# Optimization experiments

Measured on AMD Instinct MI355X. Metric: run time of the kernel, lower is better.

The kernel has to match this reference:

```python
import jax, jax.numpy as jnp
import numpy as np

# dims
B, L, D, H, HD, V, FF, NL = 1, 1024, 1024, 16, 64, 32000, 2816, 2
THETA = 500000.0
EPS = 1e-5
BOI, EOI = 31998, 31999
NEG = jnp.float32(-1e30)  # stands in for -inf in the additive mask


def setup_inputs() -> dict:
    key = jax.random.key(0)
    ks = jax.random.split(key, 12)
    tokens = jax.random.randint(ks[0], (B, L), 0, 31998)
    # inject two well-formed image spans per sequence (boi .. eoi)
    tokens = tokens.at[:, 100].set(BOI).at[:, 300].set(EOI)
    tokens = tokens.at[:, 500].set(BOI).at[:, 800].set(EOI)
    s = 0.02
    n = lambda k, shape: (jax.random.normal(k, shape, jnp.float32) * s)
    return {
        "tokens": tokens,
        "tok_emb": n(ks[1], (V, D)),
        "wq": n(ks[2], (NL, D, D)),
        "wk": n(ks[3], (NL, D, D)),
        "wv": n(ks[4], (NL, D, D)),
        "wo": n(ks[5], (NL, D, D)),
        "w1": n(ks[6], (NL, FF, D)),
        "w2": n(ks[7], (NL, D, FF)),
        "w3": n(ks[8], (NL, FF, D)),
        "attn_norm_w": jnp.ones((NL, D), jnp.float32),
        "ffn_norm_w": jnp.ones((NL, D), jnp.float32),
        "final_norm_w": jnp.ones((D,), jnp.float32),
        "w_out": n(ks[9], (V, D)),
    }


def rmsnorm(x, w):
    xf = x.astype(jnp.float32)
    y = xf * jax.lax.rsqrt(jnp.mean(xf * xf, axis=-1, keepdims=True) + EPS)
    return y.astype(x.dtype) * w


def rope_cos_sin():
    inv = 1.0 / (THETA ** (jnp.arange(0, HD, 2, dtype=jnp.float32) / HD))  # [HD/2]
    ang = jnp.arange(L, dtype=jnp.float32)[:, None] * inv[None, :]        # [L, HD/2]
    return jnp.cos(ang), jnp.sin(ang)


def apply_rope(x, cos, sin):
    # x: [B, L, H, HD]; pairs (even, odd) rotated by complex freqs_cis
    xr = x.astype(jnp.float32).reshape(B, L, H, HD // 2, 2)
    xe, xo = xr[..., 0], xr[..., 1]
    c = cos[None, :, None, :]
    s = sin[None, :, None, :]
    out = jnp.stack([xe * c - xo * s, xe * s + xo * c], axis=-1).reshape(B, L, H, HD)
    return out.astype(x.dtype)


def transfusion_mask(tokens):
    # causal everywhere + fully bidirectional within each boi..eoi span
    is_boi = tokens == BOI
    is_eoi = tokens == EOI
    boi_cnt = jnp.cumsum(is_boi.astype(jnp.int32), axis=1)          # inclusive
    eoi_before = jnp.cumsum(is_eoi.astype(jnp.int32), axis=1) - is_eoi.astype(jnp.int32)
    in_span = boi_cnt > eoi_before                                   # [B, L]
    same_span = (in_span[:, :, None] & in_span[:, None, :]) & (
        boi_cnt[:, :, None] == boi_cnt[:, None, :]
    )
    causal = jnp.arange(L)[:, None] >= jnp.arange(L)[None, :]        # [L, L]
    allowed = causal[None] | same_span                                # [B, L, L]
    return jnp.where(allowed, jnp.float32(0.0), NEG)


def reference(tokens, tok_emb, wq, wk, wv, wo, w1, w2, w3,
              attn_norm_w, ffn_norm_w, final_norm_w, w_out):
    h = tok_emb[tokens]                                # [B, L, D]
    cos, sin = rope_cos_sin()
    mask = transfusion_mask(tokens)[:, None]           # [B, 1, L, L]
    scale = 1.0 / jnp.sqrt(jnp.float32(HD))
    for l in range(NL):
        xn = rmsnorm(h, attn_norm_w[l])
        q = (xn @ wq[l].T).reshape(B, L, H, HD)
        k = (xn @ wk[l].T).reshape(B, L, H, HD)
        v = (xn @ wv[l].T).reshape(B, L, H, HD)
        q = apply_rope(q, cos, sin)
        k = apply_rope(k, cos, sin)
        q, k, v = (t.transpose(0, 2, 1, 3) for t in (q, k, v))  # [B, H, L, HD]
        scores = jnp.einsum("bhqd,bhkd->bhqk", q, k) * scale + mask
        p = jax.nn.softmax(scores.astype(jnp.float32), axis=-1).astype(q.dtype)
        attn = jnp.einsum("bhqk,bhkd->bhqd", p, v)
        attn = attn.transpose(0, 2, 1, 3).reshape(B, L, D)
        h = h + attn @ wo[l].T
        xn = rmsnorm(h, ffn_norm_w[l])
        h = h + (jax.nn.silu(xn @ w1[l].T) * (xn @ w3[l].T)) @ w2[l].T
    logits = rmsnorm(h, final_norm_w) @ w_out.T        # [B, L, V]
    return logits
```

## Files before the change

### kernel.cpp

```cpp
#include <hip/hip_runtime.h>
#include <hip/hip_bf16.h>
#include <stdint.h>

typedef unsigned short u16;
typedef __bf16 bf16x8 __attribute__((ext_vector_type(8)));
typedef u16 u16x8 __attribute__((ext_vector_type(8)));
typedef float f32x4 __attribute__((ext_vector_type(4)));

#define SEQ   1024
#define DM    1024
#define NHEADS 16
#define HDIM  64
#define VOC   32000
#define FFD   2816
#define NLAY  2

__device__ __forceinline__ u16 f2b(float f) {
    unsigned x = __builtin_bit_cast(unsigned, f);
    unsigned r = x + 0x7fffu + ((x >> 16) & 1u);
    return (u16)(r >> 16);
}
__device__ __forceinline__ float b2f(u16 u) {
    unsigned x = ((unsigned)u) << 16;
    return __builtin_bit_cast(float, x);
}
__device__ __forceinline__ float grpmax16(float v) {
    v = fmaxf(v, __shfl_xor(v, 1)); v = fmaxf(v, __shfl_xor(v, 2));
    v = fmaxf(v, __shfl_xor(v, 4)); v = fmaxf(v, __shfl_xor(v, 8));
    return v;
}
__device__ __forceinline__ float grpsum16(float v) {
    v += __shfl_xor(v, 1); v += __shfl_xor(v, 2);
    v += __shfl_xor(v, 4); v += __shfl_xor(v, 8);
    return v;
}

__device__ __forceinline__ void gll16(const void* g, void* l) {
    __builtin_amdgcn_global_load_lds(
        (__attribute__((address_space(1))) void*)(uintptr_t)g,
        (__attribute__((address_space(3))) void*)(uint32_t)(uintptr_t)l,
        16, 0, 0);
}
template <int N> __device__ __forceinline__ void vwait() {
    if constexpr (N == 0)       asm volatile("s_waitcnt vmcnt(0)" ::: "memory");
    else if constexpr (N == 4)  asm volatile("s_waitcnt vmcnt(4)" ::: "memory");
    else if constexpr (N == 8)  asm volatile("s_waitcnt vmcnt(8)" ::: "memory");
    else if constexpr (N == 10) asm volatile("s_waitcnt vmcnt(10)" ::: "memory");
    else if constexpr (N == 16) asm volatile("s_waitcnt vmcnt(16)" ::: "memory");
}
__device__ __forceinline__ int xcd_swz(int bid, int nwg) {
    const int q = nwg >> 3, r = nwg & 7;
    const int xcd = bid & 7, j = bid >> 3;
    const int start = (xcd < r) ? xcd * (q + 1) : r * (q + 1) + (xcd - r) * q;
    return start + j;
}

struct CvtArgs { const float* s[8]; u16* d[8]; int cum[9]; };
__global__ __launch_bounds__(256) void cvt_all_kernel(CvtArgs a) {
    const int stride = gridDim.x * 256;
    const int total = a.cum[8];
    for (int u = blockIdx.x * 256 + threadIdx.x; u < total; u += stride) {
        int g = 0;
#pragma unroll
        for (int k = 1; k < 8; ++k) g += (u >= a.cum[k]) ? 1 : 0;
        const int local = u - a.cum[g];
        const float4* sp = (const float4*)a.s[g] + (size_t)local * 4;
        const float4 x0 = sp[0], x1 = sp[1], x2 = sp[2], x3 = sp[3];
        ushort4 p0, p1, p2, p3;
        p0.x = f2b(x0.x); p0.y = f2b(x0.y); p0.z = f2b(x0.z); p0.w = f2b(x0.w);
        p1.x = f2b(x1.x); p1.y = f2b(x1.y); p1.z = f2b(x1.z); p1.w = f2b(x1.w);
        p2.x = f2b(x2.x); p2.y = f2b(x2.y); p2.z = f2b(x2.z); p2.w = f2b(x2.w);
        p3.x = f2b(x3.x); p3.y = f2b(x3.y); p3.z = f2b(x3.z); p3.w = f2b(x3.w);
        ushort4* dp = (ushort4*)a.d[g] + (size_t)local * 4;
        dp[0] = p0; dp[1] = p1; dp[2] = p2; dp[3] = p3;
    }
}

__global__ __launch_bounds__(256) void embed_kernel(const int* __restrict__ tok,
    const float* __restrict__ emb, float* __restrict__ h) {
    const int l = blockIdx.x;
    const int t = tok[l];
    ((float4*)(h + (size_t)l * DM))[threadIdx.x] =
        ((const float4*)(emb + (size_t)t * DM))[threadIdx.x];
}

__global__ __launch_bounds__(256) void ropetab_kernel(float* __restrict__ cosb,
                                                      float* __restrict__ sinb) {
    const int idx = blockIdx.x * 256 + threadIdx.x;
    const int l = idx >> 5, j = idx & 31;
    const float inv = __expf(-((float)j * (1.0f / 32.0f)) * 13.122363377404328f);
    const float ang = (float)l * inv;
    cosb[idx] = cosf(ang);
    sinb[idx] = sinf(ang);
}

__global__ void span_kernel(const int* __restrict__ tok, int* __restrict__ span,
                            int* __restrict__ tmask) {
    __shared__ int sb[SEQ], se[SEQ];
    __shared__ int tm[SEQ / 64];
    const int t = threadIdx.x;
    const int v = tok[t];
    const int bo = (v == 31998) ? 1 : 0;
    const int eo = (v == 31999) ? 1 : 0;
    sb[t] = bo; se[t] = eo;
    if (t < SEQ / 64) tm[t] = 0;
    __syncthreads();
    for (int o = 1; o < SEQ; o <<= 1) {
        int a = 0, b = 0;
        if (t >= o) { a = sb[t - o]; b = se[t - o]; }
        __syncthreads();
        sb[t] += a; se[t] += b;
        __syncthreads();
    }
    const int bc = sb[t];
    const int ec = se[t] - eo;
    const int id = (bc > ec) ? bc : 0;
    span[t] = id;
    if (id > 0) atomicOr(&tm[t >> 6], 1 << ((id - 1) & 31));
    __syncthreads();
    if (t < SEQ / 64) tmask[t] = tm[t];
}

__global__ __launch_bounds__(256) void rmsnorm_kernel(const float* __restrict__ x,
    const float* __restrict__ w, u16* __restrict__ o) {
    const int row = blockIdx.x;
    const float4 xv = ((const float4*)(x + (size_t)row * DM))[threadIdx.x];
    float ss = xv.x * xv.x + xv.y * xv.y + xv.z * xv.z + xv.w * xv.w;
    for (int off = 32; off; off >>= 1) ss += __shfl_xor(ss, off);
    __shared__ float red[4];
    const int lane = threadIdx.x & 63, wvi = threadIdx.x >> 6;
    if (lane == 0) red[wvi] = ss;
    __syncthreads();
    const float tot = red[0] + red[1] + red[2] + red[3];
    const float sc = rsqrtf(tot * (1.0f / (float)DM) + 1e-5f);
    const float4 wv4 = ((const float4*)w)[threadIdx.x];
    ushort4 ov;
    ov.x = f2b(xv.x * sc * wv4.x);
    ov.y = f2b(xv.y * sc * wv4.y);
    ov.z = f2b(xv.z * sc * wv4.z);
    ov.w = f2b(xv.w * sc * wv4.w);
    ((ushort4*)(o + (size_t)row * DM))[threadIdx.x] = ov;
}


template <int RESID, int BM, int BN>
__global__ __launch_bounds__(256) void gemm_p_kernel(const u16* __restrict__ A,
    const u16* __restrict__ B, float* __restrict__ C, const float* __restrict__ res,
    int N, int K) {
    constexpr int AL = BM / 32, BL = BN / 32, LOADS = AL + BL;
    constexpr int MF = BM / 32, NF = BN / 32;
    __shared__ __align__(16) u16 sA[2][BM * 64];
    __shared__ __align__(16) u16 sB[2][BN * 64];
    const int nwg = gridDim.x * gridDim.y;
    const int lid = xcd_swz(blockIdx.y * gridDim.x + blockIdx.x, nwg);
    const int tm = (lid % gridDim.x) * BM, tn = (lid / gridDim.x) * BN;
    const int tid = threadIdx.x, lane = tid & 63, wid = tid >> 6;
    const int wm = wid >> 1, wn = wid & 1, fr = lane & 15, g = lane >> 4;

    const u16* ap[AL]; const u16* bp[BL];
#pragma unroll
    for (int j = 0; j < AL; ++j) {
        const int idx = j * 256 + tid, r = idx >> 3, gr = (idx & 7) ^ (r & 7);
        ap[j] = A + (size_t)(tm + r) * K + gr * 8;
    }
#pragma unroll
    for (int j = 0; j < BL; ++j) {
        const int idx = j * 256 + tid, r = idx >> 3, gr = (idx & 7) ^ (r & 7);
        bp[j] = B + (size_t)(tn + r) * K + gr * 8;
    }

    f32x4 acc[MF][NF] = {};
    const int NT = K >> 6;
#pragma unroll
    for (int j = 0; j < AL; ++j) gll16(ap[j], &sA[0][(j * 256 + tid) * 8]);
#pragma unroll
    for (int j = 0; j < BL; ++j) gll16(bp[j], &sB[0][(j * 256 + tid) * 8]);

    int p = 0;
    for (int t = 0; t < NT; ++t) {
        if (t + 1 < NT) {
#pragma unroll
            for (int j = 0; j < AL; ++j) gll16(ap[j] + (t + 1) * 64, &sA[p ^ 1][(j * 256 + tid) * 8]);
#pragma unroll
            for (int j = 0; j < BL; ++j) gll16(bp[j] + (t + 1) * 64, &sB[p ^ 1][(j * 256 + tid) * 8]);
            vwait<LOADS>();
        } else {
            vwait<0>();
        }
        __builtin_amdgcn_s_barrier();
        __builtin_amdgcn_sched_barrier(0);
        bf16x8 af[MF][2], bfv[NF][2];
#pragma unroll
        for (int m = 0; m < MF; ++m)
#pragma unroll
            for (int ks = 0; ks < 2; ++ks) {
                const int row = wm * (BM / 2) + m * 16 + fr;
                const int gr = (ks * 4 + g) ^ (row & 7);
                af[m][ks] = *(const bf16x8*)&sA[p][row * 64 + gr * 8];
            }
#pragma unroll
        for (int n = 0; n < NF; ++n)
#pragma unroll
            for (int ks = 0; ks < 2; ++ks) {
                const int row = wn * (BN / 2) + n * 16 + fr;
                const int gr = (ks * 4 + g) ^ (row & 7);
                bfv[n][ks] = *(const bf16x8*)&sB[p][row * 64 + gr * 8];
            }
        __builtin_amdgcn_s_setprio(1);
#pragma unroll
        for (int m = 0; m < MF; ++m)
#pragma unroll
            for (int n = 0; n < NF; ++n)
#pragma unroll
                for (int ks = 0; ks < 2; ++ks)
                    acc[m][n] = __builtin_amdgcn_mfma_f32_16x16x32_bf16(af[m][ks], bfv[n][ks], acc[m][n], 0, 0, 0);
        __builtin_amdgcn_s_setprio(0);
        __builtin_amdgcn_s_barrier();
        p ^= 1;
    }

    const int cr = (lane >> 4) * 4, cc = lane & 15;
#pragma unroll
    for (int m = 0; m < MF; ++m)
#pragma unroll
        for (int n = 0; n < NF; ++n) {
            const int row0 = tm + wm * (BM / 2) + m * 16 + cr;
            const int col = tn + wn * (BN / 2) + n * 16 + cc;
#pragma unroll
            for (int r = 0; r < 4; ++r) {
                const size_t idx = (size_t)(row0 + r) * N + col;
                float v = acc[m][n][r];
                if (RESID) v += res[idx];
                C[idx] = v;
            }
        }
}

template <int RESID>
__global__ __launch_bounds__(512, 2) void gemm_big_kernel(const u16* __restrict__ A,
    const u16* __restrict__ B, float* __restrict__ C, const float* __restrict__ res,
    int N, int K) {
    __shared__ __align__(16) u16 sA[2][256 * 64];
    __shared__ __align__(16) u16 sB[2][256 * 64];
    const int nwg = gridDim.x * gridDim.y;
    const int lid = xcd_swz(blockIdx.y * gridDim.x + blockIdx.x, nwg);
    const int tm = (lid % gridDim.x) * 256;
    const int tn = (lid / gridDim.x) * 256;
    const int tid = threadIdx.x, lane = tid & 63, wid = tid >> 6;
    const int wm = wid >> 2, wn = wid & 3;
    const int fr = lane & 15, g = lane >> 4;

    const u16* ap[4]; const u16* bp[4];
#pragma unroll
    for (int j = 0; j < 4; ++j) {
        const int idx = j * 512 + tid, r = idx >> 3, gr = (idx & 7) ^ (r & 7);
        ap[j] = A + (size_t)(tm + r) * K + gr * 8;
        bp[j] = B + (size_t)(tn + r) * K + gr * 8;
    }

    f32x4 acc[8][4] = {};
    const int NT = K >> 6;
#pragma unroll
    for (int j = 0; j < 4; ++j) gll16(ap[j], &sA[0][(j * 512 + tid) * 8]);
#pragma unroll
    for (int j = 0; j < 4; ++j) gll16(bp[j], &sB[0][(j * 512 + tid) * 8]);

    int p = 0;
    for (int t = 0; t < NT; ++t) {
        if (t + 1 < NT) {
#pragma unroll
            for (int j = 0; j < 4; ++j) gll16(ap[j] + (t + 1) * 64, &sA[p ^ 1][(j * 512 + tid) * 8]);
#pragma unroll
            for (int j = 0; j < 4; ++j) gll16(bp[j] + (t + 1) * 64, &sB[p ^ 1][(j * 512 + tid) * 8]);
            vwait<8>();
        } else {
            vwait<0>();
        }
        __builtin_amdgcn_s_barrier();
        __builtin_amdgcn_sched_barrier(0);
        bf16x8 bfv[4][2];
#pragma unroll
        for (int mq = 0; mq < 4; ++mq) {
            if (mq == 0) {
#pragma unroll
                for (int n = 0; n < 4; ++n)
#pragma unroll
                    for (int ks = 0; ks < 2; ++ks) {
                        const int row = wn * 64 + n * 16 + fr;
                        const int gr = (ks * 4 + g) ^ (row & 7);
                        bfv[n][ks] = *(const bf16x8*)&sB[p][row * 64 + gr * 8];
                    }
            }
            bf16x8 af[2][2];
#pragma unroll
            for (int i = 0; i < 2; ++i)
#pragma unroll
                for (int ks = 0; ks < 2; ++ks) {
                    const int row = wm * 128 + (mq * 2 + i) * 16 + fr;
                    const int gr = (ks * 4 + g) ^ (row & 7);
                    af[i][ks] = *(const bf16x8*)&sA[p][row * 64 + gr * 8];
                }
            __builtin_amdgcn_s_setprio(1);
#pragma unroll
            for (int i = 0; i < 2; ++i)
#pragma unroll
                for (int n = 0; n < 4; ++n)
#pragma unroll
                    for (int ks = 0; ks < 2; ++ks)
                        acc[mq * 2 + i][n] = __builtin_amdgcn_mfma_f32_16x16x32_bf16(
                            af[i][ks], bfv[n][ks], acc[mq * 2 + i][n], 0, 0, 0);
            __builtin_amdgcn_s_setprio(0);
            __builtin_amdgcn_s_barrier();
        }
        p ^= 1;
    }

    const int cr = (lane >> 4) * 4, cc = lane & 15;
#pragma unroll
    for (int m = 0; m < 8; ++m)
#pragma unroll
        for (int n = 0; n < 4; ++n) {
            const int row0 = tm + wm * 128 + m * 16 + cr;
            const int col = tn + wn * 64 + n * 16 + cc;
#pragma unroll
            for (int r = 0; r < 4; ++r) {
                const size_t idx = (size_t)(row0 + r) * N + col;
                float v = acc[m][n][r];
                if (RESID) v += res[idx];
                C[idx] = v;
            }
        }
}

__global__ __launch_bounds__(256) void qkv_kernel(const u16* __restrict__ A,
    const u16* __restrict__ Bq, const u16* __restrict__ Bk, const u16* __restrict__ Bv,
    const float* __restrict__ cosb, const float* __restrict__ sinb,
    u16* __restrict__ qb, u16* __restrict__ kb, u16* __restrict__ vb) {
    __shared__ __align__(16) u16 sA[2][128 * 64];
    __shared__ __align__(16) u16 sB[2][128 * 64];
    const int lid = xcd_swz(blockIdx.y * gridDim.x + blockIdx.x, 8 * 24);
    const int tm = (lid % 8) * 128;
    const int yy = lid / 8;
    const int mat = yy >> 3;
    const int tn = (yy & 7) * 128;
    const u16* B = (mat == 0) ? Bq : (mat == 1) ? Bk : Bv;
    u16* out = (mat == 0) ? qb : (mat == 1) ? kb : vb;
    const int tid = threadIdx.x, lane = tid & 63, wid = tid >> 6;
    const int wm = wid >> 1, wn = wid & 1, fr = lane & 15, g = lane >> 4;

    const u16* ap[4]; const u16* bp[4];
#pragma unroll
    for (int j = 0; j < 4; ++j) {
        const int idx = j * 256 + tid, r = idx >> 3, gr = (idx & 7) ^ (r & 7);
        ap[j] = A + (size_t)(tm + r) * DM + gr * 8;
        bp[j] = B + (size_t)(tn + r) * DM + gr * 8;
    }

    f32x4 acc[4][4] = {};
#pragma unroll
    for (int j = 0; j < 4; ++j) gll16(ap[j], &sA[0][(j * 256 + tid) * 8]);
#pragma unroll
    for (int j = 0; j < 4; ++j) gll16(bp[j], &sB[0][(j * 256 + tid) * 8]);

    int p = 0;
    for (int t = 0; t < DM / 64; ++t) {
        if (t + 1 < DM / 64) {
#pragma unroll
            for (int j = 0; j < 4; ++j) gll16(ap[j] + (t + 1) * 64, &sA[p ^ 1][(j * 256 + tid) * 8]);
#pragma unroll
            for (int j = 0; j < 4; ++j) gll16(bp[j] + (t + 1) * 64, &sB[p ^ 1][(j * 256 + tid) * 8]);
            vwait<8>();
        } else {
            vwait<0>();
        }
        __builtin_amdgcn_s_barrier();
        __builtin_amdgcn_sched_barrier(0);
        bf16x8 af[4][2], bfv[4][2];
#pragma unroll
        for (int m = 0; m < 4; ++m)
#pragma unroll
            for (int ks = 0; ks < 2; ++ks) {
                const int row = wm * 64 + m * 16 + fr;
                const int gr = (ks * 4 + g) ^ (row & 7);
                af[m][ks] = *(const bf16x8*)&sA[p][row * 64 + gr * 8];
            }
#pragma unroll
        for (int n = 0; n < 4; ++n)
#pragma unroll
            for (int ks = 0; ks < 2; ++ks) {
                const int row = wn * 64 + n * 16 + fr;
                const int gr = (ks * 4 + g) ^ (row & 7);
                bfv[n][ks] = *(const bf16x8*)&sB[p][row * 64 + gr * 8];
            }
        __builtin_amdgcn_s_setprio(1);
#pragma unroll
        for (int m = 0; m < 4; ++m)
#pragma unroll
            for (int n = 0; n < 4; ++n)
#pragma unroll
                for (int ks = 0; ks < 2; ++ks)
                    acc[m][n] = __builtin_amdgcn_mfma_f32_16x16x32_bf16(af[m][ks], bfv[n][ks], acc[m][n], 0, 0, 0);
        __builtin_amdgcn_s_setprio(0);
        __builtin_amdgcn_s_barrier();
        p ^= 1;
    }

    const int cr = (lane >> 4) * 4, cc = lane & 15;
    if (mat < 2) {
#pragma unroll
        for (int m = 0; m < 4; ++m)
#pragma unroll
            for (int n = 0; n < 4; ++n) {
                const int row0 = tm + wm * 64 + m * 16 + cr;
                const int col = tn + wn * 64 + n * 16 + cc;
                const int j = (n * 16 + cc) >> 1;
#pragma unroll
                for (int r = 0; r < 4; ++r) {
                    const int row = row0 + r;
                    const float c = cosb[row * 32 + j];
                    const float s = sinb[row * 32 + j];
                    const float v = acc[m][n][r];
                    const float pv = __shfl_xor(v, 1);
                    const float o = (cc & 1) ? (pv * s + v * c) : (v * c - pv * s);
                    out[(size_t)row * DM + col] = f2b(o);
                }
            }
    } else {
#pragma unroll
        for (int m = 0; m < 4; ++m)
#pragma unroll
            for (int n = 0; n < 4; ++n) {
                const int row0 = tm + wm * 64 + m * 16 + cr;
                const int col = tn + wn * 64 + n * 16 + cc;
#pragma unroll
                for (int r = 0; r < 4; ++r)
                    out[(size_t)(row0 + r) * DM + col] = f2b(acc[m][n][r]);
            }
    }
}

__global__ __launch_bounds__(256) void ffn13_kernel(const u16* __restrict__ A,
    const u16* __restrict__ B1, const u16* __restrict__ B3, u16* __restrict__ Z) {
    __shared__ __align__(16) u16 sA[2][64 * 64];
    __shared__ __align__(16) u16 sB1[2][128 * 64];
    __shared__ __align__(16) u16 sB3[2][128 * 64];
    const int lid = xcd_swz(blockIdx.y * gridDim.x + blockIdx.x, 16 * 22);
    const int tm = (lid % 16) * 64;
    const int tn = (lid / 16) * 128;
    const int tid = threadIdx.x, lane = tid & 63, wid = tid >> 6;
    const int wm = wid >> 1, wn = wid & 1, fr = lane & 15, g = lane >> 4;

    const u16* ap[2]; const u16* b1p[4]; const u16* b3p[4];
#pragma unroll
    for (int j = 0; j < 2; ++j) {
        const int idx = j * 256 + tid, r = idx >> 3, gr = (idx & 7) ^ (r & 7);
        ap[j] = A + (size_t)(tm + r) * DM + gr * 8;
    }
#pragma unroll
    for (int j = 0; j < 4; ++j) {
        const int idx = j * 256 + tid, r = idx >> 3, gr = (idx & 7) ^ (r & 7);
        b1p[j] = B1 + (size_t)(tn + r) * DM + gr * 8;
        b3p[j] = B3 + (size_t)(tn + r) * DM + gr * 8;
    }

    f32x4 acc1[2][4] = {}, acc3[2][4] = {};
#pragma unroll
    for (int j = 0; j < 2; ++j) gll16(ap[j], &sA[0][(j * 256 + tid) * 8]);
#pragma unroll
    for (int j = 0; j < 4; ++j) gll16(b1p[j], &sB1[0][(j * 256 + tid) * 8]);
#pragma unroll
    for (int j = 0; j < 4; ++j) gll16(b3p[j], &sB3[0][(j * 256 + tid) * 8]);

    int p = 0;
    for (int t = 0; t < DM / 64; ++t) {
        if (t + 1 < DM / 64) {
#pragma unroll
            for (int j = 0; j < 2; ++j) gll16(ap[j] + (t + 1) * 64, &sA[p ^ 1][(j * 256 + tid) * 8]);
#pragma unroll
            for (int j = 0; j < 4; ++j) gll16(b1p[j] + (t + 1) * 64, &sB1[p ^ 1][(j * 256 + tid) * 8]);
#pragma unroll
            for (int j = 0; j < 4; ++j) gll16(b3p[j] + (t + 1) * 64, &sB3[p ^ 1][(j * 256 + tid) * 8]);
            vwait<10>();
        } else {
            vwait<0>();
        }
        __builtin_amdgcn_s_barrier();
        __builtin_amdgcn_sched_barrier(0);
        bf16x8 af[2][2], b1v[4][2], b3v[4][2];
#pragma unroll
        for (int m = 0; m < 2; ++m)
#pragma unroll
            for (int ks = 0; ks < 2; ++ks) {
                const int row = wm * 32 + m * 16 + fr;
                const int gr = (ks * 4 + g) ^ (row & 7);
                af[m][ks] = *(const bf16x8*)&sA[p][row * 64 + gr * 8];
            }
#pragma unroll
        for (int n = 0; n < 4; ++n)
#pragma unroll
            for (int ks = 0; ks < 2; ++ks) {
                const int row = wn * 64 + n * 16 + fr;
                const int gr = (ks * 4 + g) ^ (row & 7);
                b1v[n][ks] = *(const bf16x8*)&sB1[p][row * 64 + gr * 8];
                b3v[n][ks] = *(const bf16x8*)&sB3[p][row * 64 + gr * 8];
            }
        __builtin_amdgcn_s_setprio(1);
#pragma unroll
        for (int m = 0; m < 2; ++m)
#pragma unroll
            for (int n = 0; n < 4; ++n)
#pragma unroll
                for (int ks = 0; ks < 2; ++ks) {
                    acc1[m][n] = __builtin_amdgcn_mfma_f32_16x16x32_bf16(af[m][ks], b1v[n][ks], acc1[m][n], 0, 0, 0);
                    acc3[m][n] = __builtin_amdgcn_mfma_f32_16x16x32_bf16(af[m][ks], b3v[n][ks], acc3[m][n], 0, 0, 0);
                }
        __builtin_amdgcn_s_setprio(0);
        __builtin_amdgcn_s_barrier();
        p ^= 1;
    }

    const int cr = (lane >> 4) * 4, cc = lane & 15;
#pragma unroll
    for (int m = 0; m < 2; ++m)
#pragma unroll
        for (int n = 0; n < 4; ++n) {
            const int row0 = tm + wm * 32 + m * 16 + cr;
            const int col = tn + wn * 64 + n * 16 + cc;
#pragma unroll
            for (int r = 0; r < 4; ++r) {
                const float a1 = acc1[m][n][r];
                const float a3 = acc3[m][n][r];
                const float z = a1 / (1.f + __expf(-a1)) * a3;
                Z[(size_t)(row0 + r) * FFD + col] = f2b(z);
            }
        }
}

__global__ __launch_bounds__(256) void fattn_kernel(const u16* __restrict__ qb,
    const u16* __restrict__ kb, const u16* __restrict__ vb,
    const int* __restrict__ span, const int* __restrict__ tmask, u16* __restrict__ ob) {
    __shared__ __align__(16) u16 sK[64][72];
    __shared__ __align__(16) u16 sVT[64][72];
    __shared__ __align__(16) u16 sP[4][16][72];
    const int tid = threadIdx.x, lane = tid & 63, wq = tid >> 6;
    const int g = lane >> 4, fr = lane & 15;
    const int head = blockIdx.y;
    const int qbase = blockIdx.x * 64;
    const int qmask = tmask[blockIdx.x];

    bf16x8 qfr[2];
    {
        const u16* qp = qb + (size_t)(qbase + wq * 16 + fr) * DM + head * HDIM + g * 8;
        qfr[0] = *(const bf16x8*)(qp);
        qfr[1] = *(const bf16x8*)(qp + 32);
    }
    int sq[4];
#pragma unroll
    for (int r = 0; r < 4; ++r) sq[r] = span[qbase + wq * 16 + g * 4 + r];

    float m_old[4] = {-1e30f, -1e30f, -1e30f, -1e30f};
    float lsum[4] = {0.f, 0.f, 0.f, 0.f};
    f32x4 acc[4] = {};

    for (int kt = 0; kt < SEQ / 64; ++kt) {
        const int kb0 = kt * 64;
        if (kb0 > qbase && (qmask & tmask[kt]) == 0) continue;
        __syncthreads();
        {
            const int r = tid >> 2, c0 = (tid & 3) * 16;
            const u16* src = kb + (size_t)(kb0 + r) * DM + head * HDIM + c0;
            *(u16x8*)&sK[r][c0]     = *(const u16x8*)(src);
            *(u16x8*)&sK[r][c0 + 8] = *(const u16x8*)(src + 8);
        }
        {
            const int k = tid & 63, d0 = (tid >> 6) * 16;
            const u16* src = vb + (size_t)(kb0 + k) * DM + head * HDIM + d0;
            const u16x8 v0 = *(const u16x8*)(src);
            const u16x8 v1 = *(const u16x8*)(src + 8);
#pragma unroll
            for (int j = 0; j < 8; ++j) {
                sVT[d0 + j][k]     = v0[j];
                sVT[d0 + 8 + j][k] = v1[j];
            }
        }
        __syncthreads();

        f32x4 accs[4] = {};
        __builtin_amdgcn_s_setprio(1);
#pragma unroll
        for (int nf = 0; nf < 4; ++nf)
#pragma unroll
            for (int kf = 0; kf < 2; ++kf) {
                const bf16x8 kfv = *(const bf16x8*)&sK[nf * 16 + fr][g * 8 + kf * 32];
                accs[nf] = __builtin_amdgcn_mfma_f32_16x16x32_bf16(qfr[kf], kfv, accs[nf], 0, 0, 0);
            }
        __builtin_amdgcn_s_setprio(0);

        float sv[4][4]; bool al[4][4];
        if (kb0 + 63 <= qbase) {
#pragma unroll
            for (int nf = 0; nf < 4; ++nf)
#pragma unroll
                for (int r = 0; r < 4; ++r) {
                    al[nf][r] = true;
                    sv[nf][r] = accs[nf][r] * 0.125f;
                }
        } else {
            int spk[4];
#pragma unroll
            for (int nf = 0; nf < 4; ++nf) spk[nf] = span[kb0 + nf * 16 + fr];
#pragma unroll
            for (int nf = 0; nf < 4; ++nf) {
                const int key = kb0 + nf * 16 + fr;
#pragma unroll
                for (int r = 0; r < 4; ++r) {
                    const int q = qbase + wq * 16 + g * 4 + r;
                    al[nf][r] = (key <= q) || (sq[r] > 0 && spk[nf] == sq[r]);
                    sv[nf][r] = al[nf][r] ? accs[nf][r] * 0.125f : -1e30f;
                }
            }
        }
        float alpha[4], ls[4];
#pragma unroll
        for (int r = 0; r < 4; ++r) {
            float mn = fmaxf(fmaxf(sv[0][r], sv[1][r]), fmaxf(sv[2][r], sv[3][r]));
            mn = grpmax16(mn);
            const float mnew = fmaxf(m_old[r], mn);
            alpha[r] = __expf(m_old[r] - mnew);
            m_old[r] = mnew;
            ls[r] = 0.f;
        }
        u16 pb[4][4];
#pragma unroll
        for (int nf = 0; nf < 4; ++nf)
#pragma unroll
            for (int r = 0; r < 4; ++r) {
                const float p = al[nf][r] ? __expf(sv[nf][r] - m_old[r]) : 0.f;
                ls[r] += p;
                pb[nf][r] = f2b(p);
            }
#pragma unroll
        for (int r = 0; r < 4; ++r) {
            lsum[r] = lsum[r] * alpha[r] + grpsum16(ls[r]);
#pragma unroll
            for (int nf = 0; nf < 4; ++nf) acc[nf][r] *= alpha[r];
        }
#pragma unroll
        for (int nf = 0; nf < 4; ++nf)
#pragma unroll
            for (int r = 0; r < 4; ++r)
                sP[wq][g * 4 + r][nf * 16 + fr] = pb[nf][r];

        __builtin_amdgcn_s_setprio(1);
#pragma unroll
        for (int nf = 0; nf < 4; ++nf)
#pragma unroll
            for (int kf = 0; kf < 2; ++kf) {
                const bf16x8 pa  = *(const bf16x8*)&sP[wq][fr][g * 8 + kf * 32];
                const bf16x8 vtb = *(const bf16x8*)&sVT[nf * 16 + fr][g * 8 + kf * 32];
                acc[nf] = __builtin_amdgcn_mfma_f32_16x16x32_bf16(pa, vtb, acc[nf], 0, 0, 0);
            }
        __builtin_amdgcn_s_setprio(0);
    }

#pragma unroll
    for (int nf = 0; nf < 4; ++nf)
#pragma unroll
        for (int r = 0; r < 4; ++r) {
            const int q = qbase + wq * 16 + g * 4 + r;
            const int d = nf * 16 + fr;
            ob[(size_t)q * DM + head * HDIM + d] = f2b(acc[nf][r] / lsum[r]);
        }
}

extern "C" void kernel_launch(void* const* d_in, const int* in_sizes, int n_in,
                              void* d_out, int out_size, void* d_ws, size_t ws_size,
                              hipStream_t stream) {
    (void)in_sizes; (void)n_in; (void)out_size; (void)ws_size;
    const int*   tokens   = (const int*)d_in[0];
    const float* tok_emb  = (const float*)d_in[1];
    const float* wq       = (const float*)d_in[2];
    const float* wk       = (const float*)d_in[3];
    const float* wvw      = (const float*)d_in[4];
    const float* wo       = (const float*)d_in[5];
    const float* w1       = (const float*)d_in[6];
    const float* w2       = (const float*)d_in[7];
    const float* w3       = (const float*)d_in[8];
    const float* attn_nw  = (const float*)d_in[9];
    const float* ffn_nw   = (const float*)d_in[10];
    const float* final_nw = (const float*)d_in[11];
    const float* w_out    = (const float*)d_in[12];
    float* logits = (float*)d_out;

    char* ws = (char*)d_ws;
    size_t off = 0;
    auto alloc = [&](size_t b) { size_t o = off; off += (b + 255) & ~(size_t)255; return o; };
    float* h    = (float*)(ws + alloc((size_t)SEQ * DM * 4));
    u16*   xn   = (u16*)  (ws + alloc((size_t)SEQ * DM * 2));
    u16*   qb   = (u16*)  (ws + alloc((size_t)SEQ * DM * 2));
    u16*   kb   = (u16*)  (ws + alloc((size_t)SEQ * DM * 2));
    u16*   vb   = (u16*)  (ws + alloc((size_t)SEQ * DM * 2));
    u16*   ab   = (u16*)  (ws + alloc((size_t)SEQ * DM * 2));
    u16*   zb   = (u16*)  (ws + alloc((size_t)SEQ * FFD * 2));
    float* cosb = (float*)(ws + alloc((size_t)SEQ * 32 * 4));
    float* sinb = (float*)(ws + alloc((size_t)SEQ * 32 * 4));
    int*   span = (int*)  (ws + alloc((size_t)SEQ * 4));
    int*   tmask= (int*)  (ws + alloc((size_t)(SEQ / 64) * 4));
    const size_t nQ = (size_t)NLAY * DM * DM;
    const size_t nF = (size_t)NLAY * FFD * DM;
    const size_t nO = (size_t)VOC * DM;
    u16* wqb = (u16*)(ws + alloc(nQ * 2));
    u16* wkb = (u16*)(ws + alloc(nQ * 2));
    u16* wvb = (u16*)(ws + alloc(nQ * 2));
    u16* wob = (u16*)(ws + alloc(nQ * 2));
    u16* w1b = (u16*)(ws + alloc(nF * 2));
    u16* w2b = (u16*)(ws + alloc(nF * 2));
    u16* w3b = (u16*)(ws + alloc(nF * 2));
    u16* woub = (u16*)(ws + alloc(nO * 2));

    CvtArgs ca;
    const float* srcs[8] = {wq, wk, wvw, wo, w1, w2, w3, w_out};
    u16* dsts[8] = {wqb, wkb, wvb, wob, w1b, w2b, w3b, woub};
    const size_t cnts[8] = {nQ, nQ, nQ, nQ, nF, nF, nF, nO};
    int cum = 0;
    for (int i = 0; i < 8; ++i) {
        ca.s[i] = srcs[i]; ca.d[i] = dsts[i]; ca.cum[i] = cum;
        cum += (int)(cnts[i] / 16);
    }
    ca.cum[8] = cum;
    cvt_all_kernel<<<2048, 256, 0, stream>>>(ca);

    embed_kernel<<<SEQ, 256, 0, stream>>>(tokens, tok_emb, h);
    ropetab_kernel<<<(SEQ * 32) / 256, 256, 0, stream>>>(cosb, sinb);
    span_kernel<<<1, SEQ, 0, stream>>>(tokens, span, tmask);

    for (int l = 0; l < NLAY; ++l) {
        rmsnorm_kernel<<<SEQ, 256, 0, stream>>>(h, attn_nw + (size_t)l * DM, xn);
        qkv_kernel<<<dim3(8, 24), 256, 0, stream>>>(
            xn, wqb + (size_t)l * DM * DM, wkb + (size_t)l * DM * DM, wvb + (size_t)l * DM * DM,
            cosb, sinb, qb, kb, vb);
        fattn_kernel<<<dim3(SEQ / 64, NHEADS), 256, 0, stream>>>(qb, kb, vb, span, tmask, ab);
        gemm_p_kernel<1, 64, 64><<<dim3(16, 16), 256, 0, stream>>>(
            ab, wob + (size_t)l * DM * DM, h, h, DM, DM);

        rmsnorm_kernel<<<SEQ, 256, 0, stream>>>(h, ffn_nw + (size_t)l * DM, xn);
        ffn13_kernel<<<dim3(16, 22), 256, 0, stream>>>(
            xn, w1b + (size_t)l * FFD * DM, w3b + (size_t)l * FFD * DM, zb);
        gemm_p_kernel<1, 64, 64><<<dim3(16, 16), 256, 0, stream>>>(
            zb, w2b + (size_t)l * DM * FFD, h, h, DM, FFD);
    }

    rmsnorm_kernel<<<SEQ, 256, 0, stream>>>(h, final_nw, xn);
    gemm_big_kernel<0><<<dim3(SEQ / 256, VOC / 256), 512, 0, stream>>>(
        xn, woub, logits, nullptr, VOC, DM);
}
```

Before: 382.4 us.

## Fuse w_out fp32-to-bf16 conversion into the logits GEMM B-tile loads

The logits GEMM now reads the fp32 output projection weights directly, converting them to bf16 in registers and storing the swizzled result into shared memory. The separate conversion pass over the 32000x1024 weight, with its bf16 write and later re-read, is dropped. In exchange the GEMM loads twice the bytes for B through regular loads instead of async global-to-LDS copies. The conversion stores are interleaved into the MFMA loop, and a full __syncthreads is added per K step.

New measurement: 356.1 us. 1.07x faster.

```diff
diff --git a/kernel.cpp b/kernel.cpp
--- a/kernel.cpp
+++ b/kernel.cpp
@@ -142,7 +142,6 @@
     ((ushort4*)(o + (size_t)row * DM))[threadIdx.x] = ov;
 }
 
-
 template <int RESID, int BM, int BN>
 __global__ __launch_bounds__(256) void gemm_p_kernel(const u16* __restrict__ A,
     const u16* __restrict__ B, float* __restrict__ C, const float* __restrict__ res,
@@ -238,7 +237,7 @@
 
 template <int RESID>
 __global__ __launch_bounds__(512, 2) void gemm_big_kernel(const u16* __restrict__ A,
-    const u16* __restrict__ B, float* __restrict__ C, const float* __restrict__ res,
+    const float* __restrict__ B, float* __restrict__ C, const float* __restrict__ res,
     int N, int K) {
     __shared__ __align__(16) u16 sA[2][256 * 64];
     __shared__ __align__(16) u16 sB[2][256 * 64];
@@ -250,34 +249,53 @@
     const int wm = wid >> 2, wn = wid & 3;
     const int fr = lane & 15, g = lane >> 4;
 
-    const u16* ap[4]; const u16* bp[4];
+    const u16* ap[4];
 #pragma unroll
     for (int j = 0; j < 4; ++j) {
         const int idx = j * 512 + tid, r = idx >> 3, gr = (idx & 7) ^ (r & 7);
         ap[j] = A + (size_t)(tm + r) * K + gr * 8;
+    }
+    const float* bp[4];
+    int bst[4];
+#pragma unroll
+    for (int j = 0; j < 4; ++j) {
+        const int G = j * 512 + tid, r = G >> 3, gr = G & 7;
         bp[j] = B + (size_t)(tn + r) * K + gr * 8;
-    }
+        bst[j] = r * 64 + ((gr ^ (r & 7)) * 8);
+    }
+
+    auto cvtst = [&](int b, int j, const float4& x0, const float4& x1) {
+        bf16x8 v;
+        v[0] = (__bf16)x0.x; v[1] = (__bf16)x0.y; v[2] = (__bf16)x0.z; v[3] = (__bf16)x0.w;
+        v[4] = (__bf16)x1.x; v[5] = (__bf16)x1.y; v[6] = (__bf16)x1.z; v[7] = (__bf16)x1.w;
+        *(bf16x8*)&sB[b][bst[j]] = v;
+    };
 
     f32x4 acc[8][4] = {};
     const int NT = K >> 6;
-#pragma unroll
-    for (int j = 0; j < 4; ++j) gll16(ap[j], &sA[0][(j * 512 + tid) * 8]);
-#pragma unroll
-    for (int j = 0; j < 4; ++j) gll16(bp[j], &sB[0][(j * 512 + tid) * 8]);
+
+    {
+#pragma unroll
+        for (int j = 0; j < 4; ++j) gll16(ap[j], &sA[0][(j * 512 + tid) * 8]);
+        float4 b0 = *(const float4*)(bp[0]), b1 = *(const float4*)(bp[0] + 4);
+        float4 b2 = *(const float4*)(bp[1]), b3 = *(const float4*)(bp[1] + 4);
+        cvtst(0, 0, b0, b1); cvtst(0, 1, b2, b3);
+        b0 = *(const float4*)(bp[2]); b1 = *(const float4*)(bp[2] + 4);
+        b2 = *(const float4*)(bp[3]); b3 = *(const float4*)(bp[3] + 4);
+        cvtst(0, 2, b0, b1); cvtst(0, 3, b2, b3);
+        __syncthreads();
+    }
 
     int p = 0;
     for (int t = 0; t < NT; ++t) {
-        if (t + 1 < NT) {
+        const bool pre = (t + 1 < NT);
+        float4 b0, b1, b2, b3;
+        if (pre) {
 #pragma unroll
             for (int j = 0; j < 4; ++j) gll16(ap[j] + (t + 1) * 64, &sA[p ^ 1][(j * 512 + tid) * 8]);
-#pragma unroll
-            for (int j = 0; j < 4; ++j) gll16(bp[j] + (t + 1) * 64, &sB[p ^ 1][(j * 512 + tid) * 8]);
-            vwait<8>();
-        } else {
-            vwait<0>();
-        }
-        __builtin_amdgcn_s_barrier();
-        __builtin_amdgcn_sched_barrier(0);
+            b0 = *(const float4*)(bp[0] + (t + 1) * 64); b1 = *(const float4*)(bp[0] + (t + 1) * 64 + 4);
+            b2 = *(const float4*)(bp[1] + (t + 1) * 64); b3 = *(const float4*)(bp[1] + (t + 1) * 64 + 4);
+        }
         bf16x8 bfv[4][2];
 #pragma unroll
         for (int mq = 0; mq < 4; ++mq) {
@@ -290,6 +308,11 @@
                         const int gr = (ks * 4 + g) ^ (row & 7);
                         bfv[n][ks] = *(const bf16x8*)&sB[p][row * 64 + gr * 8];
                     }
+            }
+            if (mq == 2 && pre) {
+                cvtst(p ^ 1, 0, b0, b1); cvtst(p ^ 1, 1, b2, b3);
+                b0 = *(const float4*)(bp[2] + (t + 1) * 64); b1 = *(const float4*)(bp[2] + (t + 1) * 64 + 4);
+                b2 = *(const float4*)(bp[3] + (t + 1) * 64); b3 = *(const float4*)(bp[3] + (t + 1) * 64 + 4);
             }
             bf16x8 af[2][2];
 #pragma unroll
@@ -310,8 +333,10 @@
                         acc[mq * 2 + i][n] = __builtin_amdgcn_mfma_f32_16x16x32_bf16(
                             af[i][ks], bfv[n][ks], acc[mq * 2 + i][n], 0, 0, 0);
             __builtin_amdgcn_s_setprio(0);
-            __builtin_amdgcn_s_barrier();
-        }
+            if (mq < 3) __builtin_amdgcn_s_barrier();
+        }
+        if (pre) { cvtst(p ^ 1, 2, b0, b1); cvtst(p ^ 1, 3, b2, b3); }
+        __syncthreads();
         p ^= 1;
     }
 
@@ -708,7 +733,6 @@
     int*   tmask= (int*)  (ws + alloc((size_t)(SEQ / 64) * 4));
     const size_t nQ = (size_t)NLAY * DM * DM;
     const size_t nF = (size_t)NLAY * FFD * DM;
-    const size_t nO = (size_t)VOC * DM;
     u16* wqb = (u16*)(ws + alloc(nQ * 2));
     u16* wkb = (u16*)(ws + alloc(nQ * 2));
     u16* wvb = (u16*)(ws + alloc(nQ * 2));
@@ -716,18 +740,18 @@
     u16* w1b = (u16*)(ws + alloc(nF * 2));
     u16* w2b = (u16*)(ws + alloc(nF * 2));
     u16* w3b = (u16*)(ws + alloc(nF * 2));
-    u16* woub = (u16*)(ws + alloc(nO * 2));
 
     CvtArgs ca;
-    const float* srcs[8] = {wq, wk, wvw, wo, w1, w2, w3, w_out};
-    u16* dsts[8] = {wqb, wkb, wvb, wob, w1b, w2b, w3b, woub};
-    const size_t cnts[8] = {nQ, nQ, nQ, nQ, nF, nF, nF, nO};
+    const float* srcs[7] = {wq, wk, wvw, wo, w1, w2, w3};
+    u16* dsts[7] = {wqb, wkb, wvb, wob, w1b, w2b, w3b};
+    const size_t cnts[7] = {nQ, nQ, nQ, nQ, nF, nF, nF};
     int cum = 0;
-    for (int i = 0; i < 8; ++i) {
+    for (int i = 0; i < 7; ++i) {
         ca.s[i] = srcs[i]; ca.d[i] = dsts[i]; ca.cum[i] = cum;
         cum += (int)(cnts[i] / 16);
     }
-    ca.cum[8] = cum;
+    ca.s[7] = wq; ca.d[7] = wqb;
+    ca.cum[7] = cum; ca.cum[8] = cum;
     cvt_all_kernel<<<2048, 256, 0, stream>>>(ca);
 
     embed_kernel<<<SEQ, 256, 0, stream>>>(tokens, tok_emb, h);
@@ -752,5 +776,5 @@
 
     rmsnorm_kernel<<<SEQ, 256, 0, stream>>>(h, final_nw, xn);
     gemm_big_kernel<0><<<dim3(SEQ / 256, VOC / 256), 512, 0, stream>>>(
-        xn, woub, logits, nullptr, VOC, DM);
-}
+        xn, w_out, logits, nullptr, VOC, DM);
+}
```
